# Performance work log

Measured on AMD Instinct MI355X. Metric: run time of the kernel, lower is better.

## Reference

```python
import jax, jax.numpy as jnp
import numpy as np

N, D = 131072, 256   # pixels (H*W), backbone feature dim
C, K = 19, 50        # num_classes, pca_dim


def setup_inputs() -> dict:
    key = jax.random.key(0)
    k1, k2, k3, k4, k5, k6 = jax.random.split(key, 6)
    feats = jax.random.normal(k1, (N, D), dtype=jnp.float32)
    pca_mean = jax.random.normal(k2, (C, D), dtype=jnp.float32)
    pca_components = jax.random.normal(k3, (C, K, D), dtype=jnp.float32) / np.sqrt(D)
    # explained variances: strictly positive
    pca_var = jax.random.uniform(k4, (C, K), dtype=jnp.float32, minval=0.5, maxval=1.5)
    mu_c = jax.random.normal(k5, (C, K), dtype=jnp.float32)
    # SPD inverse-covariance per class
    A = jax.random.normal(k6, (C, K, K), dtype=jnp.float32)
    cov_inv = jnp.einsum('cij,ckj->cik', A, A) / K + jnp.eye(K, dtype=jnp.float32)[None]
    return {
        'feats': feats,
        'pca_mean': pca_mean,
        'pca_components': pca_components,
        'pca_var': pca_var,
        'mu_c': mu_c,
        'cov_inv': cov_inv,
        'H': 256,
        'W': 512,
    }


def reference(feats, pca_mean, pca_components, pca_var, mu_c, cov_inv, H, W):
    # Whitened PCA transform per class: (x - mean) @ comps.T / sqrt(var)
    # Avoid materializing [C, N, D]: project feats once, subtract projected mean.
    proj = jnp.einsum('nd,ckd->cnk', feats, pca_components)          # [C, N, K]
    mean_proj = jnp.einsum('cd,ckd->ck', pca_mean, pca_components)   # [C, K]
    white = (proj - mean_proj[:, None, :]) / jnp.sqrt(pca_var)[:, None, :]
    # Mahalanobis quadratic form against class Gaussian
    diff = white - mu_c[:, None, :]                                  # [C, N, K]
    dists = jnp.einsum('cnk,ckl,cnl->cn', diff, cov_inv, diff)       # [C, N]
    min_dists = jnp.min(dists, axis=0)                               # [N]
    return min_dists.reshape(H, W)
```

## Files before the change

kernel.cpp:

```cpp
#include <hip/hip_runtime.h>
#include <float.h>
#include <math.h>

constexpr int Cc = 19;
constexpr int Kk = 50;
constexpr int Dd = 256;

constexpr int NCOL = 64;
constexpr int CPAD = 20;
constexpr int ROWS = CPAD * NCOL;
constexpr int MT   = 128;
constexpr int THR  = 512;

typedef float  f32x4  __attribute__((ext_vector_type(4)));
typedef short  bf16x8 __attribute__((ext_vector_type(8)));

__device__ __forceinline__ unsigned short f2bf(float x) {
  unsigned u = __float_as_uint(x);
  unsigned r = 0x7FFFu + ((u >> 16) & 1u);
  return (unsigned short)((u + r) >> 16);
}
__device__ __forceinline__ float bf2f(unsigned short h) {
  return __uint_as_float(((unsigned)h) << 16);
}

__global__ __launch_bounds__(256) void prepchol_kernel(
    const float* __restrict__ pca_mean,
    const float* __restrict__ comps,
    const float* __restrict__ var,
    const float* __restrict__ mu,
    const float* __restrict__ cov_inv,
    float* __restrict__ w_rv,
    float* __restrict__ Lmat,
    float* __restrict__ g) {
  __shared__ float M[Kk * Kk];
  __shared__ float bcs[Kk];
  const int c = blockIdx.x, t = threadIdx.x;

  if (t < Kk) {
    const float* m  = pca_mean + (size_t)c * Dd;
    const float* cp = comps + ((size_t)(c * Kk + t)) * Dd;
    float s = 0.f;
    #pragma unroll 8
    for (int d = 0; d < Dd; ++d) s = fmaf(m[d], cp[d], s);
    float rv = 1.0f / sqrtf(var[c * Kk + t]);
    w_rv[c * Kk + t] = rv;
    bcs[t] = fmaf(s, rv, mu[c * Kk + t]);
  }
  for (int i = t; i < Kk * Kk; i += 256) M[i] = cov_inv[(size_t)c * Kk * Kk + i];
  __syncthreads();
  for (int j = 0; j < Kk; ++j) {
    if (t == 0) M[j * Kk + j] = sqrtf(M[j * Kk + j]);
    __syncthreads();
    float dj = M[j * Kk + j];
    for (int i = j + 1 + t; i < Kk; i += 256) M[i * Kk + j] /= dj;
    __syncthreads();
    const int rem = Kk - 1 - j;
    for (int idx = t; idx < rem * rem; idx += 256) {
      const int i = j + 1 + idx / rem;
      const int l = j + 1 + idx % rem;
      if (l <= i) M[i * Kk + l] -= M[i * Kk + j] * M[l * Kk + j];
    }
    __syncthreads();
  }
  for (int i = t; i < Kk * Kk; i += 256) Lmat[(size_t)c * Kk * Kk + i] = M[i];
  float s = 0.f;
  if (t < Kk) {
    for (int k = t; k < Kk; ++k) s = fmaf(M[k * Kk + t], bcs[k], s);
  }
  if (t < NCOL) g[c * NCOL + t] = s;
}

__global__ void prepB_kernel(const float* __restrict__ comps,
                             const float* __restrict__ w_rv,
                             const float* __restrict__ Lmat,
                             float* __restrict__ g,
                             unsigned short* __restrict__ Bs) {
  const int r = blockIdx.x;
  const int c = r >> 6, j = r & 63;
  const int d = threadIdx.x;
  const unsigned hi_idx =
      (unsigned)(c * 16 + (d >> 5)) * 2048u + (unsigned)j * 32u + (unsigned)(d & 31);
  const unsigned lo_idx = hi_idx + 8u * 2048u;
  if (c >= Cc || j >= Kk) {
    Bs[hi_idx] = 0; Bs[lo_idx] = 0;
    if (c >= Cc && d == 0) g[r] = 1e18f;
    return;
  }
  float s = 0.f;
  for (int k = j; k < Kk; ++k)
    s = fmaf(Lmat[(size_t)c * Kk * Kk + k * Kk + j] * w_rv[c * Kk + k],
             comps[((size_t)c * Kk + k) * Dd + d], s);
  unsigned short hi = f2bf(s);
  Bs[hi_idx] = hi;
  Bs[lo_idx] = f2bf(s - bf2f(hi));
}

__global__ __launch_bounds__(THR)
__attribute__((amdgpu_waves_per_eu(3, 3)))
void mfma_kernel(const float* __restrict__ feats,
                 const unsigned short* __restrict__ Bs,
                 const float* __restrict__ g,
                 float* __restrict__ out) {
  __shared__ unsigned short sA[MT * 512];
  __shared__ unsigned sMin[MT];

  const int tid  = threadIdx.x;
  const int lane = tid & 63;
  const int wid  = tid >> 6;
  const int mh   = wid >> 2;
  const int slot = wid & 3;
  const int l15  = lane & 15;
  const int lk   = (lane >> 4) * 8;
  const size_t pxbase = (size_t)blockIdx.x * MT;

  if (tid < MT) sMin[tid] = 0x7F7FFFFFu;

  {
    const int px = tid >> 2;
    const int db = (tid & 3) * 64;
    const float4* src = (const float4*)(feats + (pxbase + px) * Dd + db);
    char* base = (char*)sA;
    #pragma unroll 4
    for (int i = 0; i < 16; ++i) {
      float4 f = src[i];
      int k = db + i * 4;
      unsigned short h0 = f2bf(f.x), h1 = f2bf(f.y), h2 = f2bf(f.z), h3 = f2bf(f.w);
      unsigned short l0 = f2bf(f.x - bf2f(h0)), l1 = f2bf(f.y - bf2f(h1));
      unsigned short l2 = f2bf(f.z - bf2f(h2)), l3 = f2bf(f.w - bf2f(h3));
      uint2 hv, lv;
      hv.x = (unsigned)h0 | ((unsigned)h1 << 16); hv.y = (unsigned)h2 | ((unsigned)h3 << 16);
      lv.x = (unsigned)l0 | ((unsigned)l1 << 16); lv.y = (unsigned)l2 | ((unsigned)l3 << 16);
      unsigned hadr = (unsigned)(px * 1024 + k * 2)         ^ ((px & 7) << 4);
      unsigned ladr = (unsigned)(px * 1024 + (256 + k) * 2) ^ ((px & 7) << 4);
      *(uint2*)(base + hadr) = hv;
      *(uint2*)(base + ladr) = lv;
    }
  }
  __syncthreads();

  unsigned rowb[4], swr[4];
  #pragma unroll
  for (int mf = 0; mf < 4; ++mf) {
    int row = mh * 64 + mf * 16 + l15;
    rowb[mf] = (unsigned)(row * 1024);
    swr[mf]  = (unsigned)((row & 7) << 4);
  }
  const char* sAc = (const char*)sA;
  const unsigned lk2 = (unsigned)(lk * 2);

  float dmin[4][4];
  #pragma unroll
  for (int mf = 0; mf < 4; ++mf)
    #pragma unroll
    for (int r = 0; r < 4; ++r) dmin[mf][r] = FLT_MAX;

  const unsigned be = (unsigned)(l15 * 32 + lk);

  #pragma unroll 1
  for (int ci = 0; ci < CPAD / 4; ++ci) {
    const int cl = ci * 4 + slot;
    if (cl >= Cc) continue;
    const unsigned short* Bb = Bs + (size_t)cl * (16 * 2048);

    float gv[4];
    #pragma unroll
    for (int nf = 0; nf < 4; ++nf) gv[nf] = g[cl * NCOL + nf * 16 + l15];

    f32x4 acc[4][4];
    #pragma unroll
    for (int mf = 0; mf < 4; ++mf)
      #pragma unroll
      for (int nf = 0; nf < 4; ++nf) acc[mf][nf] = (f32x4)0.f;

    bf16x8 b0 = *(const bf16x8*)(Bb + 0 * 512 + be);
    bf16x8 b1 = *(const bf16x8*)(Bb + 1 * 512 + be);
    bf16x8 b2 = *(const bf16x8*)(Bb + 2 * 512 + be);
    bf16x8 b3 = *(const bf16x8*)(Bb + 3 * 512 + be);

    #pragma unroll
    for (int tb = 0; tb < 8; ++tb) {
      bf16x8 n0 = *(const bf16x8*)(Bb + (tb + 1) * 2048 + 0 * 512 + be);
      bf16x8 n1 = *(const bf16x8*)(Bb + (tb + 1) * 2048 + 1 * 512 + be);
      bf16x8 n2 = *(const bf16x8*)(Bb + (tb + 1) * 2048 + 2 * 512 + be);
      bf16x8 n3 = *(const bf16x8*)(Bb + (tb + 1) * 2048 + 3 * 512 + be);
      const unsigned kh = (unsigned)(tb * 64) + lk2;
      bf16x8 cH[4], cL[4];
      #pragma unroll
      for (int mf = 0; mf < 4; ++mf)
        cH[mf] = *(const bf16x8*)(sAc + ((rowb[mf] + kh) ^ swr[mf]));
      #pragma unroll
      for (int mf = 0; mf < 4; ++mf)
        cL[mf] = *(const bf16x8*)(sAc + ((rowb[mf] + kh + 512) ^ swr[mf]));
      __builtin_amdgcn_s_setprio(1);
      #pragma unroll
      for (int mf = 0; mf < 4; ++mf) {
        acc[mf][0] = __builtin_amdgcn_mfma_f32_16x16x32_bf16(cH[mf], b0, acc[mf][0], 0, 0, 0);
        acc[mf][1] = __builtin_amdgcn_mfma_f32_16x16x32_bf16(cH[mf], b1, acc[mf][1], 0, 0, 0);
        acc[mf][2] = __builtin_amdgcn_mfma_f32_16x16x32_bf16(cH[mf], b2, acc[mf][2], 0, 0, 0);
        acc[mf][3] = __builtin_amdgcn_mfma_f32_16x16x32_bf16(cH[mf], b3, acc[mf][3], 0, 0, 0);
      }
      #pragma unroll
      for (int mf = 0; mf < 4; ++mf) {
        acc[mf][0] = __builtin_amdgcn_mfma_f32_16x16x32_bf16(cL[mf], b0, acc[mf][0], 0, 0, 0);
        acc[mf][1] = __builtin_amdgcn_mfma_f32_16x16x32_bf16(cL[mf], b1, acc[mf][1], 0, 0, 0);
        acc[mf][2] = __builtin_amdgcn_mfma_f32_16x16x32_bf16(cL[mf], b2, acc[mf][2], 0, 0, 0);
        acc[mf][3] = __builtin_amdgcn_mfma_f32_16x16x32_bf16(cL[mf], b3, acc[mf][3], 0, 0, 0);
      }
      __builtin_amdgcn_s_setprio(0);
      b0 = n0; b1 = n1; b2 = n2; b3 = n3;
      __builtin_amdgcn_sched_barrier(0);
    }

    #pragma unroll
    for (int tb = 0; tb < 8; ++tb) {
      bf16x8 n0, n1, n2, n3;
      if (tb < 7) {
        n0 = *(const bf16x8*)(Bb + (9 + tb) * 2048 + 0 * 512 + be);
        n1 = *(const bf16x8*)(Bb + (9 + tb) * 2048 + 1 * 512 + be);
        n2 = *(const bf16x8*)(Bb + (9 + tb) * 2048 + 2 * 512 + be);
        n3 = *(const bf16x8*)(Bb + (9 + tb) * 2048 + 3 * 512 + be);
      }
      const unsigned kh = (unsigned)(tb * 64) + lk2;
      bf16x8 cH[4];
      #pragma unroll
      for (int mf = 0; mf < 4; ++mf)
        cH[mf] = *(const bf16x8*)(sAc + ((rowb[mf] + kh) ^ swr[mf]));
      __builtin_amdgcn_s_setprio(1);
      #pragma unroll
      for (int mf = 0; mf < 4; ++mf) {
        acc[mf][0] = __builtin_amdgcn_mfma_f32_16x16x32_bf16(cH[mf], b0, acc[mf][0], 0, 0, 0);
        acc[mf][1] = __builtin_amdgcn_mfma_f32_16x16x32_bf16(cH[mf], b1, acc[mf][1], 0, 0, 0);
        acc[mf][2] = __builtin_amdgcn_mfma_f32_16x16x32_bf16(cH[mf], b2, acc[mf][2], 0, 0, 0);
        acc[mf][3] = __builtin_amdgcn_mfma_f32_16x16x32_bf16(cH[mf], b3, acc[mf][3], 0, 0, 0);
      }
      __builtin_amdgcn_s_setprio(0);
      if (tb < 7) { b0 = n0; b1 = n1; b2 = n2; b3 = n3; }
      __builtin_amdgcn_sched_barrier(0);
    }

    #pragma unroll
    for (int mf = 0; mf < 4; ++mf) {
      float ps0 = 0.f, ps1 = 0.f, ps2 = 0.f, ps3 = 0.f;
      #pragma unroll
      for (int nf = 0; nf < 4; ++nf) {
        float gg = gv[nf];
        float t0 = acc[mf][nf][0] - gg; ps0 = fmaf(t0, t0, ps0);
        float t1 = acc[mf][nf][1] - gg; ps1 = fmaf(t1, t1, ps1);
        float t2 = acc[mf][nf][2] - gg; ps2 = fmaf(t2, t2, ps2);
        float t3 = acc[mf][nf][3] - gg; ps3 = fmaf(t3, t3, ps3);
      }
      #pragma unroll
      for (int off = 1; off < 16; off <<= 1) {
        ps0 += __shfl_xor(ps0, off);
        ps1 += __shfl_xor(ps1, off);
        ps2 += __shfl_xor(ps2, off);
        ps3 += __shfl_xor(ps3, off);
      }
      dmin[mf][0] = fminf(dmin[mf][0], ps0);
      dmin[mf][1] = fminf(dmin[mf][1], ps1);
      dmin[mf][2] = fminf(dmin[mf][2], ps2);
      dmin[mf][3] = fminf(dmin[mf][3], ps3);
    }
  }

  if (l15 == 0) {
    #pragma unroll
    for (int mf = 0; mf < 4; ++mf)
      #pragma unroll
      for (int r = 0; r < 4; ++r) {
        int row = mh * 64 + mf * 16 + (lane >> 4) * 4 + r;
        atomicMin(&sMin[row], __float_as_uint(dmin[mf][r]));
      }
  }
  __syncthreads();
  if (tid < MT) out[pxbase + tid] = __uint_as_float(sMin[tid]);
}

extern "C" void kernel_launch(void* const* d_in, const int* in_sizes, int n_in,
                              void* d_out, int out_size, void* d_ws, size_t ws_size,
                              hipStream_t stream) {
  const float* feats    = (const float*)d_in[0];
  const float* pca_mean = (const float*)d_in[1];
  const float* comps    = (const float*)d_in[2];
  const float* var      = (const float*)d_in[3];
  const float* mu       = (const float*)d_in[4];
  const float* cov_inv  = (const float*)d_in[5];
  float* out = (float*)d_out;

  float* w_rv = (float*)d_ws;
  float* Lmat = w_rv + Cc * Kk;
  float* gv   = Lmat + Cc * Kk * Kk;
  unsigned short* Bs = (unsigned short*)(gv + ROWS);

  const int n = in_sizes[0] / Dd;

  prepchol_kernel<<<Cc, 256, 0, stream>>>(pca_mean, comps, var, mu, cov_inv,
                                          w_rv, Lmat, gv);
  prepB_kernel<<<ROWS, 256, 0, stream>>>(comps, w_rv, Lmat, gv, Bs);
  mfma_kernel<<<n / MT, THR, 0, stream>>>(feats, Bs, gv, out);
}
```

Baseline: 268.6 us.

## Switch main GEMM to 32x32x16 MFMA with fragment-native LDS and B layouts

Replaces the 16x16x32 bf16 MFMA tiling with 32x32x16 MFMAs. The B-matrix prep layout and the shared-memory feature layout are reorganized so that each lane's fragment loads are contiguous 16-byte reads, which removes the XOR swizzle. Larger MFMA tiles mean fewer instructions and fewer LDS A-fragment reads per FLOP. In exchange, 16-wide accumulators raise register pressure, so occupancy is lowered to 2 waves per EU, and the epilogue reduction now uses more shuffle steps.

```diff
diff --git a/kernel.cpp b/kernel.cpp
--- a/kernel.cpp
+++ b/kernel.cpp
@@ -12,7 +12,7 @@
 constexpr int MT   = 128;
 constexpr int THR  = 512;
 
-typedef float  f32x4  __attribute__((ext_vector_type(4)));
+typedef float  f32x16 __attribute__((ext_vector_type(16)));
 typedef short  bf16x8 __attribute__((ext_vector_type(8)));
 
 __device__ __forceinline__ unsigned short f2bf(float x) {
@@ -79,9 +79,12 @@
   const int r = blockIdx.x;
   const int c = r >> 6, j = r & 63;
   const int d = threadIdx.x;
-  const unsigned hi_idx =
-      (unsigned)(c * 16 + (d >> 5)) * 2048u + (unsigned)j * 32u + (unsigned)(d & 31);
-  const unsigned lo_idx = hi_idx + 8u * 2048u;
+  const int kc = d >> 5, ks = (d >> 4) & 1, kh = (d >> 3) & 1, e = d & 7;
+  const int cg = j >> 5, jl = j & 31;
+  const unsigned frag = (unsigned)(kc * 4 + ks * 2 + cg);
+  const unsigned lane = (unsigned)(jl + 32 * kh);
+  const unsigned hi_idx = (unsigned)c * 32768u + frag * 512u + lane * 8u + (unsigned)e;
+  const unsigned lo_idx = hi_idx + 32u * 512u;
   if (c >= Cc || j >= Kk) {
     Bs[hi_idx] = 0; Bs[lo_idx] = 0;
     if (c >= Cc && d == 0) g[r] = 1e18f;
@@ -97,7 +100,7 @@
 }
 
 __global__ __launch_bounds__(THR)
-__attribute__((amdgpu_waves_per_eu(3, 3)))
+__attribute__((amdgpu_waves_per_eu(2, 2)))
 void mfma_kernel(const float* __restrict__ feats,
                  const unsigned short* __restrict__ Bs,
                  const float* __restrict__ g,
@@ -110,103 +113,104 @@
   const int wid  = tid >> 6;
   const int mh   = wid >> 2;
   const int slot = wid & 3;
-  const int l15  = lane & 15;
-  const int lk   = (lane >> 4) * 8;
+  const int l31  = lane & 31;
+  const int kof  = lane >> 5;
   const size_t pxbase = (size_t)blockIdx.x * MT;
 
   if (tid < MT) sMin[tid] = 0x7F7FFFFFu;
 
   {
-    const int px = tid >> 2;
-    const int db = (tid & 3) * 64;
-    const float4* src = (const float4*)(feats + (pxbase + px) * Dd + db);
+    const int px  = tid >> 2;
+    const int sub = tid & 3;
+    const float4* src = (const float4*)(feats + (pxbase + px) * Dd + sub * 64);
     char* base = (char*)sA;
-    #pragma unroll 4
-    for (int i = 0; i < 16; ++i) {
-      float4 f = src[i];
-      int k = db + i * 4;
-      unsigned short h0 = f2bf(f.x), h1 = f2bf(f.y), h2 = f2bf(f.z), h3 = f2bf(f.w);
-      unsigned short l0 = f2bf(f.x - bf2f(h0)), l1 = f2bf(f.y - bf2f(h1));
-      unsigned short l2 = f2bf(f.z - bf2f(h2)), l3 = f2bf(f.w - bf2f(h3));
-      uint2 hv, lv;
+    #pragma unroll
+    for (int i = 0; i < 8; ++i) {
+      float4 f0 = src[2 * i];
+      float4 f1 = src[2 * i + 1];
+      unsigned short h0 = f2bf(f0.x), h1 = f2bf(f0.y), h2 = f2bf(f0.z), h3 = f2bf(f0.w);
+      unsigned short h4 = f2bf(f1.x), h5 = f2bf(f1.y), h6 = f2bf(f1.z), h7 = f2bf(f1.w);
+      unsigned short l0 = f2bf(f0.x - bf2f(h0)), l1 = f2bf(f0.y - bf2f(h1));
+      unsigned short l2 = f2bf(f0.z - bf2f(h2)), l3 = f2bf(f0.w - bf2f(h3));
+      unsigned short l4 = f2bf(f1.x - bf2f(h4)), l5 = f2bf(f1.y - bf2f(h5));
+      unsigned short l6 = f2bf(f1.z - bf2f(h6)), l7 = f2bf(f1.w - bf2f(h7));
+      uint4 hv, lv;
       hv.x = (unsigned)h0 | ((unsigned)h1 << 16); hv.y = (unsigned)h2 | ((unsigned)h3 << 16);
+      hv.z = (unsigned)h4 | ((unsigned)h5 << 16); hv.w = (unsigned)h6 | ((unsigned)h7 << 16);
       lv.x = (unsigned)l0 | ((unsigned)l1 << 16); lv.y = (unsigned)l2 | ((unsigned)l3 << 16);
-      unsigned hadr = (unsigned)(px * 1024 + k * 2)         ^ ((px & 7) << 4);
-      unsigned ladr = (unsigned)(px * 1024 + (256 + k) * 2) ^ ((px & 7) << 4);
-      *(uint2*)(base + hadr) = hv;
-      *(uint2*)(base + ladr) = lv;
+      lv.z = (unsigned)l4 | ((unsigned)l5 << 16); lv.w = (unsigned)l6 | ((unsigned)l7 << 16);
+      const int k8 = sub * 8 + i;
+      *(uint4*)(base + (k8 * 128 + px) * 16)        = hv;
+      *(uint4*)(base + ((k8 + 32) * 128 + px) * 16) = lv;
     }
   }
   __syncthreads();
 
-  unsigned rowb[4], swr[4];
+  const unsigned rowb16_0 = (unsigned)((mh * 64 + l31) * 16);
+  const unsigned rowb16_1 = rowb16_0 + 32 * 16;
+  const char* sAc = (const char*)sA;
+  const unsigned koff2048 = (unsigned)(kof * 2048);
+
+  float dmin[2][16];
   #pragma unroll
-  for (int mf = 0; mf < 4; ++mf) {
-    int row = mh * 64 + mf * 16 + l15;
-    rowb[mf] = (unsigned)(row * 1024);
-    swr[mf]  = (unsigned)((row & 7) << 4);
-  }
-  const char* sAc = (const char*)sA;
-  const unsigned lk2 = (unsigned)(lk * 2);
-
-  float dmin[4][4];
-  #pragma unroll
-  for (int mf = 0; mf < 4; ++mf)
-    #pragma unroll
-    for (int r = 0; r < 4; ++r) dmin[mf][r] = FLT_MAX;
-
-  const unsigned be = (unsigned)(l15 * 32 + lk);
+  for (int mf = 0; mf < 2; ++mf)
+    #pragma unroll
+    for (int r = 0; r < 16; ++r) dmin[mf][r] = FLT_MAX;
+
+  const unsigned laneB = (unsigned)(lane * 8);
 
   #pragma unroll 1
   for (int ci = 0; ci < CPAD / 4; ++ci) {
     const int cl = ci * 4 + slot;
     if (cl >= Cc) continue;
-    const unsigned short* Bb = Bs + (size_t)cl * (16 * 2048);
-
-    float gv[4];
-    #pragma unroll
-    for (int nf = 0; nf < 4; ++nf) gv[nf] = g[cl * NCOL + nf * 16 + l15];
-
-    f32x4 acc[4][4];
-    #pragma unroll
-    for (int mf = 0; mf < 4; ++mf)
-      #pragma unroll
-      for (int nf = 0; nf < 4; ++nf) acc[mf][nf] = (f32x4)0.f;
-
-    bf16x8 b0 = *(const bf16x8*)(Bb + 0 * 512 + be);
-    bf16x8 b1 = *(const bf16x8*)(Bb + 1 * 512 + be);
-    bf16x8 b2 = *(const bf16x8*)(Bb + 2 * 512 + be);
-    bf16x8 b3 = *(const bf16x8*)(Bb + 3 * 512 + be);
+    const unsigned short* Bb = Bs + (size_t)cl * 32768;
+
+    const float gv0 = g[cl * NCOL + l31];
+    const float gv1 = g[cl * NCOL + 32 + l31];
+
+    f32x16 acc[2][2];
+    #pragma unroll
+    for (int mf = 0; mf < 2; ++mf)
+      #pragma unroll
+      for (int nf = 0; nf < 2; ++nf) acc[mf][nf] = (f32x16)0.f;
+
+    bf16x8 b0 = *(const bf16x8*)(Bb + 0 * 512 + laneB);
+    bf16x8 b1 = *(const bf16x8*)(Bb + 1 * 512 + laneB);
+    bf16x8 b2 = *(const bf16x8*)(Bb + 2 * 512 + laneB);
+    bf16x8 b3 = *(const bf16x8*)(Bb + 3 * 512 + laneB);
 
     #pragma unroll
     for (int tb = 0; tb < 8; ++tb) {
-      bf16x8 n0 = *(const bf16x8*)(Bb + (tb + 1) * 2048 + 0 * 512 + be);
-      bf16x8 n1 = *(const bf16x8*)(Bb + (tb + 1) * 2048 + 1 * 512 + be);
-      bf16x8 n2 = *(const bf16x8*)(Bb + (tb + 1) * 2048 + 2 * 512 + be);
-      bf16x8 n3 = *(const bf16x8*)(Bb + (tb + 1) * 2048 + 3 * 512 + be);
-      const unsigned kh = (unsigned)(tb * 64) + lk2;
-      bf16x8 cH[4], cL[4];
-      #pragma unroll
-      for (int mf = 0; mf < 4; ++mf)
-        cH[mf] = *(const bf16x8*)(sAc + ((rowb[mf] + kh) ^ swr[mf]));
-      #pragma unroll
-      for (int mf = 0; mf < 4; ++mf)
-        cL[mf] = *(const bf16x8*)(sAc + ((rowb[mf] + kh + 512) ^ swr[mf]));
+      bf16x8 n0 = *(const bf16x8*)(Bb + ((tb + 1) * 4 + 0) * 512 + laneB);
+      bf16x8 n1 = *(const bf16x8*)(Bb + ((tb + 1) * 4 + 1) * 512 + laneB);
+      bf16x8 n2 = *(const bf16x8*)(Bb + ((tb + 1) * 4 + 2) * 512 + laneB);
+      bf16x8 n3 = *(const bf16x8*)(Bb + ((tb + 1) * 4 + 3) * 512 + laneB);
+      const unsigned kb = (unsigned)(tb * 4) * 2048u + koff2048;
+      bf16x8 aH00 = *(const bf16x8*)(sAc + kb + rowb16_0);
+      bf16x8 aH10 = *(const bf16x8*)(sAc + kb + rowb16_1);
+      bf16x8 aH01 = *(const bf16x8*)(sAc + kb + 2 * 2048 + rowb16_0);
+      bf16x8 aH11 = *(const bf16x8*)(sAc + kb + 2 * 2048 + rowb16_1);
+      bf16x8 aL00 = *(const bf16x8*)(sAc + kb + 32 * 2048 + rowb16_0);
+      bf16x8 aL10 = *(const bf16x8*)(sAc + kb + 32 * 2048 + rowb16_1);
+      bf16x8 aL01 = *(const bf16x8*)(sAc + kb + 34 * 2048 + rowb16_0);
+      bf16x8 aL11 = *(const bf16x8*)(sAc + kb + 34 * 2048 + rowb16_1);
       __builtin_amdgcn_s_setprio(1);
-      #pragma unroll
-      for (int mf = 0; mf < 4; ++mf) {
-        acc[mf][0] = __builtin_amdgcn_mfma_f32_16x16x32_bf16(cH[mf], b0, acc[mf][0], 0, 0, 0);
-        acc[mf][1] = __builtin_amdgcn_mfma_f32_16x16x32_bf16(cH[mf], b1, acc[mf][1], 0, 0, 0);
-        acc[mf][2] = __builtin_amdgcn_mfma_f32_16x16x32_bf16(cH[mf], b2, acc[mf][2], 0, 0, 0);
-        acc[mf][3] = __builtin_amdgcn_mfma_f32_16x16x32_bf16(cH[mf], b3, acc[mf][3], 0, 0, 0);
-      }
-      #pragma unroll
-      for (int mf = 0; mf < 4; ++mf) {
-        acc[mf][0] = __builtin_amdgcn_mfma_f32_16x16x32_bf16(cL[mf], b0, acc[mf][0], 0, 0, 0);
-        acc[mf][1] = __builtin_amdgcn_mfma_f32_16x16x32_bf16(cL[mf], b1, acc[mf][1], 0, 0, 0);
-        acc[mf][2] = __builtin_amdgcn_mfma_f32_16x16x32_bf16(cL[mf], b2, acc[mf][2], 0, 0, 0);
-        acc[mf][3] = __builtin_amdgcn_mfma_f32_16x16x32_bf16(cL[mf], b3, acc[mf][3], 0, 0, 0);
-      }
+      acc[0][0] = __builtin_amdgcn_mfma_f32_32x32x16_bf16(aH00, b0, acc[0][0], 0, 0, 0);
+      acc[0][1] = __builtin_amdgcn_mfma_f32_32x32x16_bf16(aH00, b1, acc[0][1], 0, 0, 0);
+      acc[1][0] = __builtin_amdgcn_mfma_f32_32x32x16_bf16(aH10, b0, acc[1][0], 0, 0, 0);
+      acc[1][1] = __builtin_amdgcn_mfma_f32_32x32x16_bf16(aH10, b1, acc[1][1], 0, 0, 0);
+      acc[0][0] = __builtin_amdgcn_mfma_f32_32x32x16_bf16(aH01, b2, acc[0][0], 0, 0, 0);
+      acc[0][1] = __builtin_amdgcn_mfma_f32_32x32x16_bf16(aH01, b3, acc[0][1], 0, 0, 0);
+      acc[1][0] = __builtin_amdgcn_mfma_f32_32x32x16_bf16(aH11, b2, acc[1][0], 0, 0, 0);
+      acc[1][1] = __builtin_amdgcn_mfma_f32_32x32x16_bf16(aH11, b3, acc[1][1], 0, 0, 0);
+      acc[0][0] = __builtin_amdgcn_mfma_f32_32x32x16_bf16(aL00, b0, acc[0][0], 0, 0, 0);
+      acc[0][1] = __builtin_amdgcn_mfma_f32_32x32x16_bf16(aL00, b1, acc[0][1], 0, 0, 0);
+      acc[1][0] = __builtin_amdgcn_mfma_f32_32x32x16_bf16(aL10, b0, acc[1][0], 0, 0, 0);
+      acc[1][1] = __builtin_amdgcn_mfma_f32_32x32x16_bf16(aL10, b1, acc[1][1], 0, 0, 0);
+      acc[0][0] = __builtin_amdgcn_mfma_f32_32x32x16_bf16(aL01, b2, acc[0][0], 0, 0, 0);
+      acc[0][1] = __builtin_amdgcn_mfma_f32_32x32x16_bf16(aL01, b3, acc[0][1], 0, 0, 0);
+      acc[1][0] = __builtin_amdgcn_mfma_f32_32x32x16_bf16(aL11, b2, acc[1][0], 0, 0, 0);
+      acc[1][1] = __builtin_amdgcn_mfma_f32_32x32x16_bf16(aL11, b3, acc[1][1], 0, 0, 0);
       __builtin_amdgcn_s_setprio(0);
       b0 = n0; b1 = n1; b2 = n2; b3 = n3;
       __builtin_amdgcn_sched_barrier(0);
@@ -216,60 +220,55 @@
     for (int tb = 0; tb < 8; ++tb) {
       bf16x8 n0, n1, n2, n3;
       if (tb < 7) {
-        n0 = *(const bf16x8*)(Bb + (9 + tb) * 2048 + 0 * 512 + be);
-        n1 = *(const bf16x8*)(Bb + (9 + tb) * 2048 + 1 * 512 + be);
-        n2 = *(const bf16x8*)(Bb + (9 + tb) * 2048 + 2 * 512 + be);
-        n3 = *(const bf16x8*)(Bb + (9 + tb) * 2048 + 3 * 512 + be);
+        n0 = *(const bf16x8*)(Bb + ((9 + tb) * 4 + 0) * 512 + laneB);
+        n1 = *(const bf16x8*)(Bb + ((9 + tb) * 4 + 1) * 512 + laneB);
+        n2 = *(const bf16x8*)(Bb + ((9 + tb) * 4 + 2) * 512 + laneB);
+        n3 = *(const bf16x8*)(Bb + ((9 + tb) * 4 + 3) * 512 + laneB);
       }
-      const unsigned kh = (unsigned)(tb * 64) + lk2;
-      bf16x8 cH[4];
-      #pragma unroll
-      for (int mf = 0; mf < 4; ++mf)
-        cH[mf] = *(const bf16x8*)(sAc + ((rowb[mf] + kh) ^ swr[mf]));
+      const unsigned kb = (unsigned)(tb * 4) * 2048u + koff2048;
+      bf16x8 aH00 = *(const bf16x8*)(sAc + kb + rowb16_0);
+      bf16x8 aH10 = *(const bf16x8*)(sAc + kb + rowb16_1);
+      bf16x8 aH01 = *(const bf16x8*)(sAc + kb + 2 * 2048 + rowb16_0);
+      bf16x8 aH11 = *(const bf16x8*)(sAc + kb + 2 * 2048 + rowb16_1);
       __builtin_amdgcn_s_setprio(1);
-      #pragma unroll
-      for (int mf = 0; mf < 4; ++mf) {
-        acc[mf][0] = __builtin_amdgcn_mfma_f32_16x16x32_bf16(cH[mf], b0, acc[mf][0], 0, 0, 0);
-        acc[mf][1] = __builtin_amdgcn_mfma_f32_16x16x32_bf16(cH[mf], b1, acc[mf][1], 0, 0, 0);
-        acc[mf][2] = __builtin_amdgcn_mfma_f32_16x16x32_bf16(cH[mf], b2, acc[mf][2], 0, 0, 0);
-        acc[mf][3] = __builtin_amdgcn_mfma_f32_16x16x32_bf16(cH[mf], b3, acc[mf][3], 0, 0, 0);
-      }
+      acc[0][0] = __builtin_amdgcn_mfma_f32_32x32x16_bf16(aH00, b0, acc[0][0], 0, 0, 0);
+      acc[0][1] = __builtin_amdgcn_mfma_f32_32x32x16_bf16(aH00, b1, acc[0][1], 0, 0, 0);
+      acc[1][0] = __builtin_amdgcn_mfma_f32_32x32x16_bf16(aH10, b0, acc[1][0], 0, 0, 0);
+      acc[1][1] = __builtin_amdgcn_mfma_f32_32x32x16_bf16(aH10, b1, acc[1][1], 0, 0, 0);
+      acc[0][0] = __builtin_amdgcn_mfma_f32_32x32x16_bf16(aH01, b2, acc[0][0], 0, 0, 0);
+      acc[0][1] = __builtin_amdgcn_mfma_f32_32x32x16_bf16(aH01, b3, acc[0][1], 0, 0, 0);
+      acc[1][0] = __builtin_amdgcn_mfma_f32_32x32x16_bf16(aH11, b2, acc[1][0], 0, 0, 0);
+      acc[1][1] = __builtin_amdgcn_mfma_f32_32x32x16_bf16(aH11, b3, acc[1][1], 0, 0, 0);
       __builtin_amdgcn_s_setprio(0);
       if (tb < 7) { b0 = n0; b1 = n1; b2 = n2; b3 = n3; }
       __builtin_amdgcn_sched_barrier(0);
     }
 
     #pragma unroll
-    for (int mf = 0; mf < 4; ++mf) {
-      float ps0 = 0.f, ps1 = 0.f, ps2 = 0.f, ps3 = 0.f;
-      #pragma unroll
-      for (int nf = 0; nf < 4; ++nf) {
-        float gg = gv[nf];
-        float t0 = acc[mf][nf][0] - gg; ps0 = fmaf(t0, t0, ps0);
-        float t1 = acc[mf][nf][1] - gg; ps1 = fmaf(t1, t1, ps1);
-        float t2 = acc[mf][nf][2] - gg; ps2 = fmaf(t2, t2, ps2);
-        float t3 = acc[mf][nf][3] - gg; ps3 = fmaf(t3, t3, ps3);
+    for (int mf = 0; mf < 2; ++mf) {
+      float ps[16];
+      #pragma unroll
+      for (int r = 0; r < 16; ++r) {
+        float t0 = acc[mf][0][r] - gv0;
+        float t1 = acc[mf][1][r] - gv1;
+        ps[r] = fmaf(t1, t1, t0 * t0);
       }
       #pragma unroll
-      for (int off = 1; off < 16; off <<= 1) {
-        ps0 += __shfl_xor(ps0, off);
-        ps1 += __shfl_xor(ps1, off);
-        ps2 += __shfl_xor(ps2, off);
-        ps3 += __shfl_xor(ps3, off);
+      for (int off = 1; off < 32; off <<= 1) {
+        #pragma unroll
+        for (int r = 0; r < 16; ++r) ps[r] += __shfl_xor(ps[r], off);
       }
-      dmin[mf][0] = fminf(dmin[mf][0], ps0);
-      dmin[mf][1] = fminf(dmin[mf][1], ps1);
-      dmin[mf][2] = fminf(dmin[mf][2], ps2);
-      dmin[mf][3] = fminf(dmin[mf][3], ps3);
-    }
-  }
-
-  if (l15 == 0) {
-    #pragma unroll
-    for (int mf = 0; mf < 4; ++mf)
-      #pragma unroll
-      for (int r = 0; r < 4; ++r) {
-        int row = mh * 64 + mf * 16 + (lane >> 4) * 4 + r;
+      #pragma unroll
+      for (int r = 0; r < 16; ++r) dmin[mf][r] = fminf(dmin[mf][r], ps[r]);
+    }
+  }
+
+  if (l31 == 0) {
+    #pragma unroll
+    for (int mf = 0; mf < 2; ++mf)
+      #pragma unroll
+      for (int r = 0; r < 16; ++r) {
+        int row = mh * 64 + mf * 32 + (r & 3) + 8 * (r >> 2) + 4 * kof;
         atomicMin(&sMin[row], __float_as_uint(dmin[mf][r]));
       }
   }
```

Result: slower. 319.0 us (+18.8%).
